# Kernel optimization log

Hardware: AMD Instinct MI355X
Metric: run time of the kernel (lower is better)

## Reference

```python
import jax, jax.numpy as jnp
import numpy as np

B, P, K, HE, HF = 256, 128, 512, 1024, 512
D = K + HE + 2 * HF  # 2560, MLP input dim
HID = 64


def setup_inputs() -> dict:
    key = jax.random.key(0)
    ks = jax.random.split(key, 6)
    query = jax.random.normal(ks[0], (B, 1, HE), dtype=jnp.float32)
    keys = jax.random.normal(ks[1], (B, P, K), dtype=jnp.float32)
    frameLSTM_h = jax.random.normal(ks[2], (B, 1, 2 * HF), dtype=jnp.float32)
    mask = jax.random.randint(ks[3], (B, P), 0, 2, dtype=jnp.int32)
    mask = mask.at[:, 0].set(1)  # guarantee at least one unmasked player per row
    W1 = jax.random.normal(ks[4], (D, HID), dtype=jnp.float32) / np.float32(np.sqrt(D))
    W2 = jax.random.normal(ks[5], (HID, 1), dtype=jnp.float32) / np.float32(np.sqrt(HID))
    return dict(query=query, keys=keys, frameLSTM_h=frameLSTM_h, mask=mask, W1=W1, W2=W2)


def reference(query, keys, frameLSTM_h, mask, W1, W2):
    # Faithful to: cat([keys, query.repeat, frame.repeat]) @ W1 -> ReLU -> @ W2.
    # The pre-activation is linear, so splitting W1 by row-blocks is exactly the
    # same math without materializing the repeated/concatenated (B,P,D) tensor.
    W1k = W1[:K]            # (K, 64)
    W1q = W1[K:K + HE]      # (HE, 64)
    W1f = W1[K + HE:]       # (2*HF, 64)
    h = jax.nn.relu(
        jnp.einsum('bpk,kh->bph', keys, W1k)
        + jnp.einsum('boe,eh->boh', query, W1q)        # broadcasts over P
        + jnp.einsum('bof,fh->boh', frameLSTM_h, W1f)  # broadcasts over P
    )  # (B, P, 64)
    raw_scores = jnp.einsum('bph,ho->bp', h, W2)  # (B, P)
    raw_scores = jnp.where(mask == 0, -jnp.inf, raw_scores)
    weights = jax.nn.softmax(raw_scores, axis=1)  # (B, P)
    context = jnp.einsum('bp,bpk->bk', weights, keys)[:, None, :]  # (B, 1, K)
    embeddings = jnp.concatenate([context, frameLSTM_h], axis=2)   # (B, 1, K+2*HF)
    return embeddings, weights
```

## Files before the change

kernel.cpp:

```cpp
#include <hip/hip_runtime.h>
#include <hip/hip_bf16.h>
#include <cstdint>
#include <math.h>


typedef __bf16 bf16;
typedef __attribute__((ext_vector_type(8))) __bf16 bf16x8;
typedef __attribute__((ext_vector_type(4))) float f32x4;

#define NB 256
#define NP 128
#define NK 512
#define SKLD 520
#define SK_BYTES (NP * SKLD * 2)
#define SMEM_BYTES (SK_BYTES + 128 * 4 + 128 * 4)

__global__ __launch_bounds__(256) void prep_kernel(
    const float* __restrict__ W1, const float* __restrict__ query,
    const float* __restrict__ frame, bf16* __restrict__ w1kt,
    float* __restrict__ proj)
{
    const int blk = blockIdx.x;
    const int t = threadIdx.x;
    if (blk < 16) {
        __shared__ float s[32][65];
        const int k0 = blk * 32;
#pragma unroll
        for (int i = 0; i < 8; i++) {
            const int idx = t + 256 * i;
            const int k = idx >> 6, h = idx & 63;
            s[k][h] = W1[(size_t)(k0 + k) * 64 + h];
        }
        __syncthreads();
#pragma unroll
        for (int i = 0; i < 8; i++) {
            const int idx = t + 256 * i;
            const int h = idx >> 5, kk = idx & 31;
            w1kt[(size_t)h * 512 + k0 + kk] = (bf16)s[kk][h];
        }
    } else {
        __shared__ float sq[4][2048];
        __shared__ float red[4][4][64];
        const int b0 = (blk - 16) * 4;

#pragma unroll
        for (int i = 0; i < 8; i++) {
            const int flat = (t + 256 * i) * 4;
            const int bl = flat >> 11;
            const int d  = flat & 2047;
            const float* src = (d < 1024)
                ? (query + (size_t)(b0 + bl) * 1024 + d)
                : (frame + (size_t)(b0 + bl) * 1024 + (d - 1024));
            *(float4*)&sq[bl][d] = *(const float4*)src;
        }
        __syncthreads();

        const int c = t >> 6;
        const int h = t & 63;
        const float* w1c = W1 + (size_t)(512 + c * 512) * 64 + h;
        float acc[4] = {0.f, 0.f, 0.f, 0.f};

        float wreg[2][16];
#pragma unroll
        for (int u = 0; u < 16; u++) wreg[0][u] = w1c[(size_t)u * 64];

#pragma unroll 2
        for (int dd = 0; dd < 512; dd += 16) {
            const int cur = (dd >> 4) & 1;
            if (dd + 16 < 512) {
#pragma unroll
                for (int u = 0; u < 16; u++)
                    wreg[cur ^ 1][u] = w1c[(size_t)(dd + 16 + u) * 64];
            }
#pragma unroll
            for (int u4 = 0; u4 < 4; u4++) {
                float4 qv[4];
#pragma unroll
                for (int j = 0; j < 4; j++)
                    qv[j] = *(const float4*)&sq[j][c * 512 + dd + u4 * 4];
#pragma unroll
                for (int uu = 0; uu < 4; uu++) {
                    const float wv = wreg[cur][u4 * 4 + uu];
                    acc[0] += (&qv[0].x)[uu] * wv;
                    acc[1] += (&qv[1].x)[uu] * wv;
                    acc[2] += (&qv[2].x)[uu] * wv;
                    acc[3] += (&qv[3].x)[uu] * wv;
                }
            }
        }
#pragma unroll
        for (int j = 0; j < 4; j++) red[c][j][h] = acc[j];
        __syncthreads();
        const int j2 = t >> 6;
        proj[(size_t)(b0 + j2) * 64 + h] =
            red[0][j2][h] + red[1][j2][h] + red[2][j2][h] + red[3][j2][h];
    }
}

__global__ __launch_bounds__(512) void attn_kernel(
    const float* __restrict__ keys, const float* __restrict__ frame,
    const int* __restrict__ mask, const float* __restrict__ W2,
    const bf16* __restrict__ w1kt, const float* __restrict__ proj,
    float* __restrict__ out)
{
    extern __shared__ char smem[];
    bf16* sk      = (bf16*)smem;
    float* scores = (float*)(smem + SK_BYTES);
    float* wts    = scores + 128;

    const int b = blockIdx.x;
    const int t = threadIdx.x;
    const int w = t >> 6;
    const int lane = t & 63;
    const int m = lane & 15;
    const int q = lane >> 4;
    const int p0 = w * 16;

    float pv[4], wv[4];
#pragma unroll
    for (int nt = 0; nt < 4; nt++) {
        pv[nt] = proj[b * 64 + nt * 16 + m];
        wv[nt] = W2[nt * 16 + m];
    }

    const float* arow = keys + (size_t)b * (NP * NK) + (size_t)(p0 + m) * NK + q * 8;
    const bf16* bb = w1kt + m * 512 + q * 8;
    bf16* swr = sk + (size_t)(p0 + m) * SKLD + q * 8;

    f32x4 acc[4];
#pragma unroll
    for (int nt = 0; nt < 4; nt++) acc[nt] = (f32x4){0.f, 0.f, 0.f, 0.f};

    float4 Aa[2], Ab[2];
    bf16x8 Bp[2][4];
    Aa[0] = *(const float4*)(arow);
    Ab[0] = *(const float4*)(arow + 4);
#pragma unroll
    for (int nt = 0; nt < 4; nt++) Bp[0][nt] = *(const bf16x8*)(bb + nt * 8192);

#pragma unroll
    for (int kk = 0; kk < 16; kk++) {
        const int cur = kk & 1;
        if (kk < 15) {
            Aa[cur ^ 1] = *(const float4*)(arow + (kk + 1) * 32);
            Ab[cur ^ 1] = *(const float4*)(arow + (kk + 1) * 32 + 4);
#pragma unroll
            for (int nt = 0; nt < 4; nt++)
                Bp[cur ^ 1][nt] = *(const bf16x8*)(bb + nt * 8192 + (kk + 1) * 32);
        }
        bf16x8 Af;
        Af[0] = (bf16)Aa[cur].x; Af[1] = (bf16)Aa[cur].y;
        Af[2] = (bf16)Aa[cur].z; Af[3] = (bf16)Aa[cur].w;
        Af[4] = (bf16)Ab[cur].x; Af[5] = (bf16)Ab[cur].y;
        Af[6] = (bf16)Ab[cur].z; Af[7] = (bf16)Ab[cur].w;
        *(bf16x8*)(swr + kk * 32) = Af;
#pragma unroll
        for (int nt = 0; nt < 4; nt++)
            acc[nt] = __builtin_amdgcn_mfma_f32_16x16x32_bf16(Af, Bp[cur][nt], acc[nt], 0, 0, 0);
    }

    float pr[4] = {0.f, 0.f, 0.f, 0.f};
#pragma unroll
    for (int nt = 0; nt < 4; nt++)
#pragma unroll
        for (int r = 0; r < 4; r++)
            pr[r] += fmaxf(acc[nt][r] + pv[nt], 0.f) * wv[nt];

#pragma unroll
    for (int off = 1; off < 16; off <<= 1)
#pragma unroll
        for (int r = 0; r < 4; r++)
            pr[r] += __shfl_xor(pr[r], off);

    if (m == 0) {
#pragma unroll
        for (int r = 0; r < 4; r++) scores[p0 + q * 4 + r] = pr[r];
    }
    __syncthreads();

    if (t < 64) {
        const int pa = t, pb = t + 64;
        float s0 = (mask[b * 128 + pa] == 0) ? -INFINITY : scores[pa];
        float s1 = (mask[b * 128 + pb] == 0) ? -INFINITY : scores[pb];
        float mx = fmaxf(s0, s1);
#pragma unroll
        for (int off = 32; off; off >>= 1) mx = fmaxf(mx, __shfl_xor(mx, off));
        float e0 = __expf(s0 - mx), e1 = __expf(s1 - mx);
        float sum = e0 + e1;
#pragma unroll
        for (int off = 32; off; off >>= 1) sum += __shfl_xor(sum, off);
        const float inv = 1.0f / sum;
        e0 *= inv; e1 *= inv;
        wts[pa] = e0; wts[pb] = e1;
        float* wout = out + (size_t)NB * 1536;
        wout[b * 128 + pa] = e0;
        wout[b * 128 + pb] = e1;
    }
    __syncthreads();

    {
        float c0 = 0.f, c1 = 0.f;
#pragma unroll 8
        for (int p = 0; p < 128; p += 2) {
            const uint32_t u0 = (uint32_t)*(const uint16_t*)(sk + (size_t)p * SKLD + t);
            const uint32_t u1 = (uint32_t)*(const uint16_t*)(sk + (size_t)(p + 1) * SKLD + t);
            c0 += wts[p] * __uint_as_float(u0 << 16);
            c1 += wts[p + 1] * __uint_as_float(u1 << 16);
        }
        out[(size_t)b * 1536 + t] = c0 + c1;
    }
    if (t < 256) {
        const float4 fv = *(const float4*)(frame + (size_t)b * 1024 + t * 4);
        *(float4*)(out + (size_t)b * 1536 + 512 + t * 4) = fv;
    }
}

extern "C" void kernel_launch(void* const* d_in, const int* in_sizes, int n_in,
                              void* d_out, int out_size, void* d_ws, size_t ws_size,
                              hipStream_t stream) {
    const float* query = (const float*)d_in[0];
    const float* keys  = (const float*)d_in[1];
    const float* frame = (const float*)d_in[2];
    const int*   mask  = (const int*)d_in[3];
    const float* W1    = (const float*)d_in[4];
    const float* W2    = (const float*)d_in[5];
    float* out = (float*)d_out;

    bf16* w1kt  = (bf16*)d_ws;
    float* proj = (float*)((char*)d_ws + (64 << 10));

    hipFuncSetAttribute((const void*)attn_kernel,
                        hipFuncAttributeMaxDynamicSharedMemorySize, SMEM_BYTES);

    prep_kernel<<<80, 256, 0, stream>>>(W1, query, frame, w1kt, proj);
    attn_kernel<<<256, 512, SMEM_BYTES, stream>>>(keys, frame, mask, W2,
                                                  w1kt, proj, out);
}
```

Baseline: 136.8 us.

## Split attention into separate scores and context kernels, re-reading keys from global

Splits the fused attention kernel in two. A scores kernel uses two blocks per batch row, with no large LDS staging of keys, to raise occupancy. A context kernel re-reads keys in fp32 from global (likely L2/MALL-resident) to compute the softmax-weighted sum. The prep kernel is reshaped to 512 threads and fewer blocks, with deeper register prefetch of W1. This trades the LDS bf16 copy of keys for a second global read of keys and an extra launch. The context sum now uses fp32 keys instead of bf16, which improves accuracy.

```diff
diff --git a/kernel.cpp b/kernel.cpp
--- a/kernel.cpp
+++ b/kernel.cpp
@@ -11,41 +11,37 @@
 #define NB 256
 #define NP 128
 #define NK 512
-#define SKLD 520
-#define SK_BYTES (NP * SKLD * 2)
-#define SMEM_BYTES (SK_BYTES + 128 * 4 + 128 * 4)
-
-__global__ __launch_bounds__(256) void prep_kernel(
+
+__global__ __launch_bounds__(512) void prep_kernel(
     const float* __restrict__ W1, const float* __restrict__ query,
     const float* __restrict__ frame, bf16* __restrict__ w1kt,
     float* __restrict__ proj)
 {
+    __shared__ float s[64][65];
+    __shared__ float sq[4][2048];
+    __shared__ float red[8][4][64];
     const int blk = blockIdx.x;
     const int t = threadIdx.x;
-    if (blk < 16) {
-        __shared__ float s[32][65];
-        const int k0 = blk * 32;
+    if (blk < 8) {
+        const int k0 = blk * 64;
 #pragma unroll
         for (int i = 0; i < 8; i++) {
-            const int idx = t + 256 * i;
+            const int idx = t + 512 * i;
             const int k = idx >> 6, h = idx & 63;
             s[k][h] = W1[(size_t)(k0 + k) * 64 + h];
         }
         __syncthreads();
 #pragma unroll
         for (int i = 0; i < 8; i++) {
-            const int idx = t + 256 * i;
-            const int h = idx >> 5, kk = idx & 31;
+            const int idx = t + 512 * i;
+            const int h = idx >> 6, kk = idx & 63;
             w1kt[(size_t)h * 512 + k0 + kk] = (bf16)s[kk][h];
         }
     } else {
-        __shared__ float sq[4][2048];
-        __shared__ float red[4][4][64];
-        const int b0 = (blk - 16) * 4;
-
-#pragma unroll
-        for (int i = 0; i < 8; i++) {
-            const int flat = (t + 256 * i) * 4;
+        const int b0 = (blk - 8) * 4;
+#pragma unroll
+        for (int i = 0; i < 4; i++) {
+            const int flat = (t + 512 * i) * 4;
             const int bl = flat >> 11;
             const int d  = flat & 2047;
             const float* src = (d < 1024)
@@ -55,29 +51,31 @@
         }
         __syncthreads();
 
-        const int c = t >> 6;
+        const int w = t >> 6;
         const int h = t & 63;
-        const float* w1c = W1 + (size_t)(512 + c * 512) * 64 + h;
+        const float* w1c = W1 + (size_t)(512 + w * 256) * 64 + h;
+        float wreg[4][16];
+#pragma unroll
+        for (int bu = 0; bu < 3; bu++)
+#pragma unroll
+            for (int u = 0; u < 16; u++)
+                wreg[bu][u] = w1c[(size_t)(bu * 16 + u) * 64];
+
         float acc[4] = {0.f, 0.f, 0.f, 0.f};
-
-        float wreg[2][16];
-#pragma unroll
-        for (int u = 0; u < 16; u++) wreg[0][u] = w1c[(size_t)u * 64];
-
-#pragma unroll 2
-        for (int dd = 0; dd < 512; dd += 16) {
-            const int cur = (dd >> 4) & 1;
-            if (dd + 16 < 512) {
+#pragma unroll
+        for (int rr = 0; rr < 16; rr++) {
+            const int cur = rr & 3;
+            if (rr < 13) {
 #pragma unroll
                 for (int u = 0; u < 16; u++)
-                    wreg[cur ^ 1][u] = w1c[(size_t)(dd + 16 + u) * 64];
+                    wreg[(rr + 3) & 3][u] = w1c[(size_t)((rr + 3) * 16 + u) * 64];
             }
 #pragma unroll
             for (int u4 = 0; u4 < 4; u4++) {
                 float4 qv[4];
 #pragma unroll
                 for (int j = 0; j < 4; j++)
-                    qv[j] = *(const float4*)&sq[j][c * 512 + dd + u4 * 4];
+                    qv[j] = *(const float4*)&sq[j][w * 256 + rr * 16 + u4 * 4];
 #pragma unroll
                 for (int uu = 0; uu < 4; uu++) {
                     const float wv = wreg[cur][u4 * 4 + uu];
@@ -89,32 +87,32 @@
             }
         }
 #pragma unroll
-        for (int j = 0; j < 4; j++) red[c][j][h] = acc[j];
+        for (int j = 0; j < 4; j++) red[w][j][h] = acc[j];
         __syncthreads();
-        const int j2 = t >> 6;
-        proj[(size_t)(b0 + j2) * 64 + h] =
-            red[0][j2][h] + red[1][j2][h] + red[2][j2][h] + red[3][j2][h];
-    }
-}
-
-__global__ __launch_bounds__(512) void attn_kernel(
-    const float* __restrict__ keys, const float* __restrict__ frame,
-    const int* __restrict__ mask, const float* __restrict__ W2,
+        if (t < 256) {
+            const int j2 = t >> 6, hh = t & 63;
+            float sum = 0.f;
+#pragma unroll
+            for (int ww = 0; ww < 8; ww++) sum += red[ww][j2][hh];
+            proj[(size_t)(b0 + j2) * 64 + hh] = sum;
+        }
+    }
+}
+
+__global__ __launch_bounds__(256, 2) void scores_kernel(
+    const float* __restrict__ keys, const float* __restrict__ W2,
     const bf16* __restrict__ w1kt, const float* __restrict__ proj,
-    float* __restrict__ out)
+    float* __restrict__ sws)
 {
-    extern __shared__ char smem[];
-    bf16* sk      = (bf16*)smem;
-    float* scores = (float*)(smem + SK_BYTES);
-    float* wts    = scores + 128;
-
-    const int b = blockIdx.x;
+    const int blk = blockIdx.x;
+    const int b = blk >> 1;
+    const int ph = blk & 1;
     const int t = threadIdx.x;
     const int w = t >> 6;
     const int lane = t & 63;
     const int m = lane & 15;
     const int q = lane >> 4;
-    const int p0 = w * 16;
+    const int p0 = ph * 64 + w * 16;
 
     float pv[4], wv[4];
 #pragma unroll
@@ -125,7 +123,6 @@
 
     const float* arow = keys + (size_t)b * (NP * NK) + (size_t)(p0 + m) * NK + q * 8;
     const bf16* bb = w1kt + m * 512 + q * 8;
-    bf16* swr = sk + (size_t)(p0 + m) * SKLD + q * 8;
 
     f32x4 acc[4];
 #pragma unroll
@@ -153,7 +150,6 @@
         Af[2] = (bf16)Aa[cur].z; Af[3] = (bf16)Aa[cur].w;
         Af[4] = (bf16)Ab[cur].x; Af[5] = (bf16)Ab[cur].y;
         Af[6] = (bf16)Ab[cur].z; Af[7] = (bf16)Ab[cur].w;
-        *(bf16x8*)(swr + kk * 32) = Af;
 #pragma unroll
         for (int nt = 0; nt < 4; nt++)
             acc[nt] = __builtin_amdgcn_mfma_f32_16x16x32_bf16(Af, Bp[cur][nt], acc[nt], 0, 0, 0);
@@ -174,14 +170,24 @@
 
     if (m == 0) {
 #pragma unroll
-        for (int r = 0; r < 4; r++) scores[p0 + q * 4 + r] = pr[r];
-    }
-    __syncthreads();
+        for (int r = 0; r < 4; r++)
+            sws[(size_t)b * 128 + p0 + q * 4 + r] = pr[r];
+    }
+}
+
+__global__ __launch_bounds__(512, 2) void ctx_kernel(
+    const float* __restrict__ keys, const float* __restrict__ frame,
+    const int* __restrict__ mask, const float* __restrict__ sws,
+    float* __restrict__ out)
+{
+    __shared__ float wts[128];
+    const int b = blockIdx.x;
+    const int t = threadIdx.x;
 
     if (t < 64) {
         const int pa = t, pb = t + 64;
-        float s0 = (mask[b * 128 + pa] == 0) ? -INFINITY : scores[pa];
-        float s1 = (mask[b * 128 + pb] == 0) ? -INFINITY : scores[pb];
+        float s0 = (mask[b * 128 + pa] == 0) ? -INFINITY : sws[(size_t)b * 128 + pa];
+        float s1 = (mask[b * 128 + pb] == 0) ? -INFINITY : sws[(size_t)b * 128 + pb];
         float mx = fmaxf(s0, s1);
 #pragma unroll
         for (int off = 32; off; off >>= 1) mx = fmaxf(mx, __shfl_xor(mx, off));
@@ -198,17 +204,25 @@
     }
     __syncthreads();
 
-    {
-        float c0 = 0.f, c1 = 0.f;
-#pragma unroll 8
-        for (int p = 0; p < 128; p += 2) {
-            const uint32_t u0 = (uint32_t)*(const uint16_t*)(sk + (size_t)p * SKLD + t);
-            const uint32_t u1 = (uint32_t)*(const uint16_t*)(sk + (size_t)(p + 1) * SKLD + t);
-            c0 += wts[p] * __uint_as_float(u0 << 16);
-            c1 += wts[p + 1] * __uint_as_float(u1 << 16);
-        }
-        out[(size_t)b * 1536 + t] = c0 + c1;
-    }
+    const float* kc = keys + (size_t)b * (NP * NK) + t;
+    float kreg[2][16];
+#pragma unroll
+    for (int i = 0; i < 16; i++) kreg[0][i] = kc[(size_t)i * NK];
+    float acc = 0.f;
+#pragma unroll
+    for (int c8 = 0; c8 < 8; c8++) {
+        const int cur = c8 & 1;
+        if (c8 < 7) {
+#pragma unroll
+            for (int i = 0; i < 16; i++)
+                kreg[cur ^ 1][i] = kc[(size_t)((c8 + 1) * 16 + i) * NK];
+        }
+#pragma unroll
+        for (int i = 0; i < 16; i++)
+            acc += wts[c8 * 16 + i] * kreg[cur][i];
+    }
+    out[(size_t)b * 1536 + t] = acc;
+
     if (t < 256) {
         const float4 fv = *(const float4*)(frame + (size_t)b * 1024 + t * 4);
         *(float4*)(out + (size_t)b * 1536 + 512 + t * 4) = fv;
@@ -228,11 +242,9 @@
 
     bf16* w1kt  = (bf16*)d_ws;
     float* proj = (float*)((char*)d_ws + (64 << 10));
-
-    hipFuncSetAttribute((const void*)attn_kernel,
-                        hipFuncAttributeMaxDynamicSharedMemorySize, SMEM_BYTES);
-
-    prep_kernel<<<80, 256, 0, stream>>>(W1, query, frame, w1kt, proj);
-    attn_kernel<<<256, 512, SMEM_BYTES, stream>>>(keys, frame, mask, W2,
-                                                  w1kt, proj, out);
-}
+    float* sws  = (float*)((char*)d_ws + (128 << 10));
+
+    prep_kernel<<<72, 512, 0, stream>>>(W1, query, frame, w1kt, proj);
+    scores_kernel<<<512, 256, 0, stream>>>(keys, W2, w1kt, proj, sws);
+    ctx_kernel<<<256, 512, 0, stream>>>(keys, frame, mask, sws, out);
+}
```

New measurement: 140.7 us. 2.8% more time.
